# Performance work log

Measured on AMD Instinct MI355X. Metric: run time of the kernel, lower is better.

The kernel has to match this reference:

```python
import jax, jax.numpy as jnp
import numpy as np

B, T, N = 32, 512, 16
C, V, D, H, L = 150, 832, 512, 512, 5  # chord vocab, note vocab, embed dim, hidden, layers


def setup_inputs() -> dict:
    key = jax.random.key(0)
    ks = jax.random.split(key, 16)
    s = 0.05
    note = jax.random.randint(ks[0], (B, T, N), 0, V)
    chord = jax.random.randint(ks[1], (B, T), 0, C)
    chord_table = jax.random.normal(ks[2], (C, D), jnp.float32) * s
    note_table = jax.random.normal(ks[3], (V, D), jnp.float32) * s
    # GRU layer 0 (input = 2*D), layers 1..L-1 (input = H), gate order r,z,n like torch
    w_ih0 = jax.random.normal(ks[4], (3 * H, 2 * D), jnp.float32) * s
    w_hh0 = jax.random.normal(ks[5], (3 * H, H), jnp.float32) * s
    b_ih0 = jax.random.normal(ks[6], (3 * H,), jnp.float32) * s
    b_hh0 = jax.random.normal(ks[7], (3 * H,), jnp.float32) * s
    w_ih_r = jax.random.normal(ks[8], (L - 1, 3 * H, H), jnp.float32) * s
    w_hh_r = jax.random.normal(ks[9], (L - 1, 3 * H, H), jnp.float32) * s
    b_ih_r = jax.random.normal(ks[10], (L - 1, 3 * H), jnp.float32) * s
    b_hh_r = jax.random.normal(ks[11], (L - 1, 3 * H), jnp.float32) * s
    fc_w = jax.random.normal(ks[12], (C, H), jnp.float32) * s
    fc_b = jax.random.normal(ks[13], (C,), jnp.float32) * s
    return dict(note=note, chord=chord, chord_table=chord_table, note_table=note_table,
                w_ih0=w_ih0, w_hh0=w_hh0, b_ih0=b_ih0, b_hh0=b_hh0,
                w_ih_r=w_ih_r, w_hh_r=w_hh_r, b_ih_r=b_ih_r, b_hh_r=b_hh_r,
                fc_w=fc_w, fc_b=fc_b)


def _gru_layer(x, wih, whh, bih, bhh):
    # x: [B, T, in] -> [B, T, H], torch GRU cell math (gate order r,z,n)
    xp = jnp.einsum('bti,gi->btg', x, wih) + bih          # precompute input proj [B,T,3H]
    xp = jnp.swapaxes(xp, 0, 1)                            # [T,B,3H]
    h0 = jnp.zeros((x.shape[0], whh.shape[1]), x.dtype)

    def step(h, xpt):
        gh = h @ whh.T + bhh
        xr, xz, xn = jnp.split(xpt, 3, axis=-1)
        hr, hz, hn = jnp.split(gh, 3, axis=-1)
        r = jax.nn.sigmoid(xr + hr)
        z = jax.nn.sigmoid(xz + hz)
        n = jnp.tanh(xn + r * hn)
        h_new = (1.0 - z) * n + z * h
        return h_new, h_new

    _, ys = jax.lax.scan(step, h0, xp)
    return jnp.swapaxes(ys, 0, 1)                          # [B,T,H]


def _forward(note, chord, chord_table, note_table, w_ih0, w_hh0, b_ih0, b_hh0,
             w_ih_r, w_hh_r, b_ih_r, b_hh_r, fc_w, fc_b):
    # padding_idx=0: zero row 0 of both tables (also blocks its gradient)
    ct = chord_table.at[0].set(0.0)
    nt = note_table.at[0].set(0.0)
    chord_emb = ct[chord]                                   # [B,T,D]
    # ragged mean over notes before first zero; mask[k]=1 iff no zero in note[...,:k+1]
    mask = jnp.cumprod((note != 0).astype(chord_table.dtype), axis=-1)  # [B,T,N]
    emb = nt[note]                                          # [B,T,N,D]
    cnt = jnp.maximum(mask.sum(-1), 1.0)                    # zero_index==0 case -> mean of zero row
    note_emb = jnp.einsum('btnd,btn->btd', emb, mask) / cnt[..., None]
    x = jnp.concatenate([chord_emb, note_emb], axis=-1)     # [B,T,2D]
    x = _gru_layer(x, w_ih0, w_hh0, b_ih0, b_hh0)
    for l in range(w_ih_r.shape[0]):
        x = _gru_layer(x, w_ih_r[l], w_hh_r[l], b_ih_r[l], b_hh_r[l])
    return x @ fc_w.T + fc_b                                # [B,T,C]


def reference(note, chord, chord_table, note_table, w_ih0, w_hh0, b_ih0, b_hh0,
              w_ih_r, w_hh_r, b_ih_r, b_hh_r, fc_w, fc_b):
    return _forward(note, chord, chord_table, note_table, w_ih0, w_hh0, b_ih0, b_hh0,
                    w_ih_r, w_hh_r, b_ih_r, b_hh_r, fc_w, fc_b)
```

## Files before the change

### kernel.cpp

```cpp
#include <hip/hip_runtime.h>
#include <hip/hip_bf16.h>

#define B_   32
#define T_   512
#define NN_  16
#define CV_  150
#define D_   512
#define H_   512
#define BT_  16384
#define K0_  1024
#define G3H_ 1536
#define NBF_ 160
#define GXB_ 6144
#define FCB_ 768
#define XSLOT_ 16384
#define XRING_ 32
#define HRING_ 8
#define SENT32 0x7f7f7f7fu
#define HCAP 16384
#define XCAP 16384
#define BCAP 65536

using bf16x8 = __attribute__((ext_vector_type(8))) short;
using f32x4  = __attribute__((ext_vector_type(4))) float;
using u32x4  = __attribute__((ext_vector_type(4))) unsigned int;
typedef unsigned long long u64;

__device__ __forceinline__ unsigned short f2bf(float f){
  unsigned int u = __builtin_bit_cast(unsigned int, f);
  u += 0x7fffu + ((u >> 16) & 1u);
  return (unsigned short)(u >> 16);
}

__device__ __forceinline__ void store8(unsigned short* p, f32x4 a, f32x4 b){
  union { unsigned short us[8]; u32x4 v; } u;
  u.us[0]=f2bf(a[0]); u.us[1]=f2bf(a[1]); u.us[2]=f2bf(a[2]); u.us[3]=f2bf(a[3]);
  u.us[4]=f2bf(b[0]); u.us[5]=f2bf(b[1]); u.us[6]=f2bf(b[2]); u.us[7]=f2bf(b[3]);
  *(u32x4*)p = u.v;
}

__device__ __forceinline__ u64 ld_coh_u64(const u64* p){
  return __hip_atomic_load(p, __ATOMIC_RELAXED, __HIP_MEMORY_SCOPE_AGENT);
}
__device__ __forceinline__ void st_coh_u32(void* p, unsigned int v){
  __hip_atomic_store((unsigned int*)p, v, __ATOMIC_RELAXED, __HIP_MEMORY_SCOPE_AGENT);
}
__device__ __forceinline__ float ld_coh_f32(const float* p){
  return __hip_atomic_load(p, __ATOMIC_RELAXED, __HIP_MEMORY_SCOPE_AGENT);
}
__device__ __forceinline__ void st_coh_f32(float* p, float v){
  __hip_atomic_store((unsigned int*)p, __builtin_bit_cast(unsigned int, v),
                     __ATOMIC_RELAXED, __HIP_MEMORY_SCOPE_AGENT);
}
__device__ __forceinline__ void st_flag(int* p, int v){
  __hip_atomic_store(p, v, __ATOMIC_RELAXED, __HIP_MEMORY_SCOPE_AGENT);
}
__device__ __forceinline__ int ld_flag(const int* p){
  return __hip_atomic_load(p, __ATOMIC_RELAXED, __HIP_MEMORY_SCOPE_AGENT);
}

__device__ __forceinline__ bool bad64(u64 q){
  return ((unsigned int)q == SENT32) | ((unsigned int)(q >> 32) == SENT32);
}

__global__ void convert_bf16(const float* __restrict__ src,
                             unsigned short* __restrict__ dst, int n){
  int i = blockIdx.x * 256 + threadIdx.x;
  if (i < n) dst[i] = f2bf(src[i]);
}

__global__ __launch_bounds__(64) void emb_kernel(
    const int* __restrict__ note, const int* __restrict__ chord,
    const float* __restrict__ ctab, const float* __restrict__ ntab,
    unsigned short* __restrict__ x0){
  const int bt = blockIdx.x;
  const int tid = threadIdx.x;
  __shared__ int sn[NN_];
  if (tid < NN_) sn[tid] = note[bt * NN_ + tid];
  __syncthreads();
  float alive = 1.f, cnt = 0.f;
  float msk[NN_];
  #pragma unroll
  for (int k = 0; k < NN_; ++k){ if (sn[k] == 0) alive = 0.f; msk[k] = alive; cnt += alive; }
  const float inv = 1.f / fmaxf(cnt, 1.f);
  const int ch = chord[bt];
  const int d0 = tid * 8;
  f32x4 c0 = {0.f,0.f,0.f,0.f}, c1 = {0.f,0.f,0.f,0.f};
  if (ch != 0){
    const float* cp = ctab + (size_t)ch * D_ + d0;
    c0 = *(const f32x4*)cp; c1 = *(const f32x4*)(cp + 4);
  }
  f32x4 s0 = {0.f,0.f,0.f,0.f}, s1 = {0.f,0.f,0.f,0.f};
  #pragma unroll
  for (int k = 0; k < NN_; ++k){
    if (msk[k] != 0.f){
      const float* np = ntab + (size_t)sn[k] * D_ + d0;
      s0 += *(const f32x4*)np;
      s1 += *(const f32x4*)(np + 4);
    }
  }
  s0 *= inv; s1 *= inv;
  unsigned short* o = x0 + (size_t)bt * K0_ + d0;
  store8(o, c0, c1);
  store8(o + D_, s0, s1);
}

union Ufrag { u64 q[2]; bf16x8 v; };

__global__ __launch_bounds__(256, 1) void gru_fused(
    float* xp, unsigned short* hT, unsigned short* xT, unsigned short* xout,
    int* cprog, const unsigned short* __restrict__ x0g,
    const unsigned short* __restrict__ wih0g, const float* __restrict__ bih0g,
    int* gprog,
    const float* __restrict__ whh0g, const float* __restrict__ whhrg,
    const float* __restrict__ wihrg, const float* __restrict__ bhh0g,
    const float* __restrict__ bihrg, const float* __restrict__ bhhrg,
    int* l4prog, const unsigned short* __restrict__ fcwbg,
    const float* __restrict__ fcbg, float* outg){
  __shared__ unsigned short w_s[96 * 512];
  __shared__ float p_s[2][4][2][2][16][16];

  const int tid = threadIdx.x;
  const int blk = blockIdx.x;

  if (blk >= NBF_ && blk < NBF_ + GXB_){
    const int idx = blk - NBF_;
    const int gx  = idx % 24;
    const int gyy = idx / 24;
    const int bb  = gyy & 31, tc = gyy >> 5;
    const int m0  = bb * 512 + tc * 64;
    const int lane = tid & 63, wave = tid >> 6;
    const int l15 = lane & 15, kq4 = lane >> 4;
    const int m_frag = m0 + wave * 16 + l15;
    const int n_base = gx * 64;
    f32x4 acc[4] = {{0.f,0.f,0.f,0.f},{0.f,0.f,0.f,0.f},{0.f,0.f,0.f,0.f},{0.f,0.f,0.f,0.f}};
    const unsigned short* xptr = x0g + (size_t)m_frag * K0_ + kq4 * 8;
    const unsigned short* wptr[4];
    #pragma unroll
    for (int i = 0; i < 4; ++i){
      int n = n_base + i * 16 + l15;
      wptr[i] = wih0g + (size_t)n * K0_ + kq4 * 8;
    }
    for (int k0 = 0; k0 < K0_; k0 += 32){
      bf16x8 a = *(const bf16x8*)(xptr + k0);
      #pragma unroll
      for (int i = 0; i < 4; ++i){
        bf16x8 b = *(const bf16x8*)(wptr[i] + k0);
        acc[i] = __builtin_amdgcn_mfma_f32_16x16x32_bf16(a, b, acc[i], 0, 0, 0);
      }
    }
    const int mrow = m0 + wave * 16 + kq4 * 4;
    #pragma unroll
    for (int i = 0; i < 4; ++i){
      int n = n_base + i * 16 + l15;
      float bv = bih0g[n];
      #pragma unroll
      for (int r = 0; r < 4; ++r){
        int m = mrow + r;
        float v = acc[i][r] + bv;
        st_coh_f32(&xp[((size_t)(m & (T_-1)) * G3H_ + n) * B_ + (m >> 9)], v);
      }
    }
    asm volatile("s_waitcnt vmcnt(0)" ::: "memory");
    __syncthreads();
    if (tid == 0) atomicAdd(&gprog[tc], 1);
    return;
  }

  if (blk >= NBF_ + GXB_){
    const int fidx = blk - NBF_ - GXB_;
    const int fx  = fidx % 3;
    const int fyy = fidx / 3;
    const int bb  = fyy & 31, tmc = fyy >> 5;
    const int m0  = bb * 512 + tmc * 64;
    const int lane = tid & 63, wave = tid >> 6;
    const int l15 = lane & 15, kq4 = lane >> 4;
    const int need = tmc * 64 + 63;
    {
      int itc = 0;
      while (true){
        int v = (lane < 32) ? ld_flag(&l4prog[lane]) : 0x7fffffff;
        if (__all(v >= need)) break;
        if (++itc > (1 << 20)) break;
        __builtin_amdgcn_s_sleep(8);
      }
    }
    __builtin_amdgcn_sched_barrier(0);
    const int m_frag = m0 + wave * 16 + l15;
    f32x4 acc[4] = {{0.f,0.f,0.f,0.f},{0.f,0.f,0.f,0.f},{0.f,0.f,0.f,0.f},{0.f,0.f,0.f,0.f}};
    const unsigned short* xptr = xout + (size_t)m_frag * H_ + kq4 * 8;
    const unsigned short* wptr[4];
    #pragma unroll
    for (int i = 0; i < 4; ++i){
      int n = fx * 64 + i * 16 + l15;
      if (n >= CV_) n = CV_ - 1;
      wptr[i] = fcwbg + (size_t)n * H_ + kq4 * 8;
    }
    for (int k0 = 0; k0 < H_; k0 += 32){
      Ufrag ua;
      const u64* sp = (const u64*)(xptr + k0);
      ua.q[0] = ld_coh_u64(sp); ua.q[1] = ld_coh_u64(sp + 1);
      bf16x8 a = ua.v;
      #pragma unroll
      for (int i = 0; i < 4; ++i){
        bf16x8 b = *(const bf16x8*)(wptr[i] + k0);
        acc[i] = __builtin_amdgcn_mfma_f32_16x16x32_bf16(a, b, acc[i], 0, 0, 0);
      }
    }
    const int mrow = m0 + wave * 16 + kq4 * 4;
    #pragma unroll
    for (int i = 0; i < 4; ++i){
      int n = fx * 64 + i * 16 + l15;
      if (n < CV_){
        float bv = fcbg[n];
        #pragma unroll
        for (int r = 0; r < 4; ++r)
          outg[(size_t)(mrow + r) * CV_ + n] = acc[i][r] + bv;
      }
    }
    return;
  }

  const int l   = blk >> 5;
  const int sub = blk & 31;

  {
    #pragma unroll 1
    for (int i = 0; i < 24; ++i){
      int idx = i * 256 + tid;
      int fr = idx >> 6, lam = idx & 63;
      int ks = fr & 31, g = fr >> 5;
      int row = g * 512 + sub * 16 + (lam & 15);
      int kcol = (ks & 15) * 32 + ((lam >> 4) << 3);
      f32x4 a = {0.f,0.f,0.f,0.f}, b2 = {0.f,0.f,0.f,0.f};
      if (l == 0){
        if (ks < 16){
          const float* sp = whh0g + (size_t)row * H_ + kcol;
          a = *(const f32x4*)sp; b2 = *(const f32x4*)(sp + 4);
        }
      } else {
        const float* wbase = (ks < 16) ? whhrg : wihrg;
        const float* sp = wbase + (size_t)(l - 1) * G3H_ * H_ + (size_t)row * H_ + kcol;
        a = *(const f32x4*)sp; b2 = *(const f32x4*)(sp + 4);
      }
      store8(&w_s[fr * 512 + lam * 8], a, b2);
    }
  }
  __syncthreads();

  const int lane = tid & 63, wave = tid >> 6;
  const int l15 = lane & 15, l4 = lane >> 4;
  const int myn = wave >> 1;
  const int kh  = wave & 1;
  const int myb = (myn << 4) + l15;
  const int fro = (l4 << 3);
  const int khofs = kh * 256;
  const int khb = kh * 8;

  const int cb = tid & 31;
  const int cj = (tid >> 5) * 2;
  const int jg = sub * 16 + cj;

  float br0, bz0, bx0, bn0, br1, bz1, bx1, bn1;
  if (l == 0){
    br0 = bhh0g[jg];       bz0 = bhh0g[512 + jg];     bx0 = 0.f; bn0 = bhh0g[1024 + jg];
    br1 = bhh0g[jg + 1];   bz1 = bhh0g[512 + jg + 1]; bx1 = 0.f; bn1 = bhh0g[1024 + jg + 1];
  } else {
    const float* bi = bihrg + (size_t)(l - 1) * G3H_;
    const float* bh = bhhrg + (size_t)(l - 1) * G3H_;
    br0 = bi[jg] + bh[jg];           bz0 = bi[512 + jg] + bh[512 + jg];
    bx0 = bi[1024 + jg];             bn0 = bh[1024 + jg];
    br1 = bi[jg + 1] + bh[jg + 1];   bz1 = bi[512 + jg + 1] + bh[512 + jg + 1];
    bx1 = bi[1024 + jg + 1];         bn1 = bh[1024 + jg + 1];
  }
  float hres0 = 0.f, hres1 = 0.f;

  unsigned short* hTl = hT + (size_t)l * (HRING_ * 32 * 512);
  unsigned short* xTw = xT + (size_t)(l < 4 ? l : 0) * ((size_t)XRING_ * XSLOT_);
  const unsigned short* xTr = xT + (size_t)(l > 0 ? l - 1 : 0) * ((size_t)XRING_ * XSLOT_);
  const int* bp_own = cprog + (l << 5);
  int*       bp_pub = cprog + ((l > 0 ? l - 1 : 0) << 5);

  float era=0,eza=0,ena=0,era1=0,eza1=0,ena1=0;
  float erb=0,ezb=0,enb=0,erb1=0,ezb1=0,enb1=0;
  if (l == 0){
    if (tid == 0){
      int itc = 0;
      while (ld_flag(&gprog[0]) < 768){
        if (++itc > (1 << 20)) break;
        __builtin_amdgcn_s_sleep(8);
      }
    }
    __syncthreads();
    { const float* xq = xp + (size_t)0 * (G3H_ * B_) + cb;
      era=ld_coh_f32(&xq[(size_t)(0*H_+jg)*B_]); era1=ld_coh_f32(&xq[(size_t)(0*H_+jg+1)*B_]);
      eza=ld_coh_f32(&xq[(size_t)(1*H_+jg)*B_]); eza1=ld_coh_f32(&xq[(size_t)(1*H_+jg+1)*B_]);
      ena=ld_coh_f32(&xq[(size_t)(2*H_+jg)*B_]); ena1=ld_coh_f32(&xq[(size_t)(2*H_+jg+1)*B_]); }
    { const float* xq = xp + (size_t)1 * (G3H_ * B_) + cb;
      erb=ld_coh_f32(&xq[(size_t)(0*H_+jg)*B_]); erb1=ld_coh_f32(&xq[(size_t)(0*H_+jg+1)*B_]);
      ezb=ld_coh_f32(&xq[(size_t)(1*H_+jg)*B_]); ezb1=ld_coh_f32(&xq[(size_t)(1*H_+jg+1)*B_]);
      enb=ld_coh_f32(&xq[(size_t)(2*H_+jg)*B_]); enb1=ld_coh_f32(&xq[(size_t)(2*H_+jg+1)*B_]); }
  }

  for (int t = 0; t < T_; ++t){
    const int pb = t & 1;

    Ufrag xb[8];
    const unsigned short* xs = nullptr;
    if (l > 0){
      xs = xTr + (size_t)(t & (XRING_-1)) * XSLOT_ + (size_t)myb * 512 + khofs + fro;
      #pragma unroll
      for (int j = 0; j < 8; ++j){
        const u64* sp = (const u64*)(xs + (j << 5));
        xb[j].q[0] = ld_coh_u64(sp); xb[j].q[1] = ld_coh_u64(sp + 1);
      }
    }

    Ufrag hb[8];
    const unsigned short* hf = hTl + (((size_t)(t & (HRING_-1)) * 32 + myb) << 9) + khofs + fro;
    #pragma unroll
    for (int j = 0; j < 8; ++j){
      const u64* sp = (const u64*)(hf + (j << 5));
      hb[j].q[0] = ld_coh_u64(sp); hb[j].q[1] = ld_coh_u64(sp + 1);
    }

    if (l < 4 && t && (t & 3) == 0){
      int itc = 0;
      while (true){
        int v = (lane < 32) ? ld_flag(&bp_own[lane]) : 0x7fffffff;
        if (__all(v >= t - 4)) break;
        if (++itc > BCAP) break;
        __builtin_amdgcn_s_sleep(2);
      }
    }

    f32x4 accR = {0.f,0.f,0.f,0.f}, accZ = {0.f,0.f,0.f,0.f};
    f32x4 accN = {0.f,0.f,0.f,0.f}, accX = {0.f,0.f,0.f,0.f};

    if (l > 0){
      #pragma unroll
      for (int j = 0; j < 8; ++j){
        int itc = 0;
        while (__any((int)(bad64(xb[j].q[0]) | bad64(xb[j].q[1])))){
          if (++itc > XCAP) break;
          if (itc > 2) __builtin_amdgcn_s_sleep(2);
          const u64* sp = (const u64*)(xs + (j << 5));
          xb[j].q[0] = ld_coh_u64(sp); xb[j].q[1] = ld_coh_u64(sp + 1);
        }
        bf16x8 b  = xb[j].v;
        bf16x8 a0 = *(const bf16x8*)&w_s[(0 * 32 + 16 + khb + j) * 512 + lane * 8];
        bf16x8 a1 = *(const bf16x8*)&w_s[(1 * 32 + 16 + khb + j) * 512 + lane * 8];
        bf16x8 a2 = *(const bf16x8*)&w_s[(2 * 32 + 16 + khb + j) * 512 + lane * 8];
        accR = __builtin_amdgcn_mfma_f32_16x16x32_bf16(a0, b, accR, 0, 0, 0);
        accZ = __builtin_amdgcn_mfma_f32_16x16x32_bf16(a1, b, accZ, 0, 0, 0);
        accX = __builtin_amdgcn_mfma_f32_16x16x32_bf16(a2, b, accX, 0, 0, 0);
      }
    }

    #pragma unroll
    for (int j = 0; j < 8; ++j){
      int itc = 0;
      while (__any((int)(bad64(hb[j].q[0]) | bad64(hb[j].q[1])))){
        if (++itc > HCAP) break;
        if (itc > 2) __builtin_amdgcn_s_sleep(2);
        const u64* sp = (const u64*)(hf + (j << 5));
        hb[j].q[0] = ld_coh_u64(sp); hb[j].q[1] = ld_coh_u64(sp + 1);
      }
      bf16x8 b  = hb[j].v;
      bf16x8 a0 = *(const bf16x8*)&w_s[(0 * 32 + khb + j) * 512 + lane * 8];
      bf16x8 a1 = *(const bf16x8*)&w_s[(1 * 32 + khb + j) * 512 + lane * 8];
      bf16x8 a2 = *(const bf16x8*)&w_s[(2 * 32 + khb + j) * 512 + lane * 8];
      accR = __builtin_amdgcn_mfma_f32_16x16x32_bf16(a0, b, accR, 0, 0, 0);
      accZ = __builtin_amdgcn_mfma_f32_16x16x32_bf16(a1, b, accZ, 0, 0, 0);
      accN = __builtin_amdgcn_mfma_f32_16x16x32_bf16(a2, b, accN, 0, 0, 0);
    }

    float erc=0,ezc=0,enc=0,erc1=0,ezc1=0,enc1=0;
    if (l == 0){
      if (((t + 2) & 63) == 0){
        const int ck = ((t + 2) & (T_ - 1)) >> 6;
        if (tid == 0){
          int itc = 0;
          while (ld_flag(&gprog[ck]) < 768){
            if (++itc > (1 << 20)) break;
            __builtin_amdgcn_s_sleep(8);
          }
        }
        __syncthreads();
      }
      const float* xq = xp + (size_t)((t + 2) & (T_ - 1)) * (G3H_ * B_) + cb;
      erc=ld_coh_f32(&xq[(size_t)(0*H_+jg)*B_]); erc1=ld_coh_f32(&xq[(size_t)(0*H_+jg+1)*B_]);
      ezc=ld_coh_f32(&xq[(size_t)(1*H_+jg)*B_]); ezc1=ld_coh_f32(&xq[(size_t)(1*H_+jg+1)*B_]);
      enc=ld_coh_f32(&xq[(size_t)(2*H_+jg)*B_]); enc1=ld_coh_f32(&xq[(size_t)(2*H_+jg+1)*B_]);
    }

    #pragma unroll
    for (int r = 0; r < 4; ++r){
      int u = l4 * 4 + r;
      p_s[pb][0][myn][kh][u][l15] = accR[r];
      p_s[pb][1][myn][kh][u][l15] = accZ[r];
      p_s[pb][2][myn][kh][u][l15] = accN[r];
      p_s[pb][3][myn][kh][u][l15] = accX[r];
    }
    __syncthreads();

    {
      const int nt = cb >> 4, bc = cb & 15;
      float rp0 = p_s[pb][0][nt][0][cj][bc]   + p_s[pb][0][nt][1][cj][bc];
      float rp1 = p_s[pb][0][nt][0][cj+1][bc] + p_s[pb][0][nt][1][cj+1][bc];
      float zp0 = p_s[pb][1][nt][0][cj][bc]   + p_s[pb][1][nt][1][cj][bc];
      float zp1 = p_s[pb][1][nt][0][cj+1][bc] + p_s[pb][1][nt][1][cj+1][bc];
      float hp0 = p_s[pb][2][nt][0][cj][bc]   + p_s[pb][2][nt][1][cj][bc];
      float hp1 = p_s[pb][2][nt][0][cj+1][bc] + p_s[pb][2][nt][1][cj+1][bc];
      float xq0 = p_s[pb][3][nt][0][cj][bc]   + p_s[pb][3][nt][1][cj][bc];
      float xq1 = p_s[pb][3][nt][0][cj+1][bc] + p_s[pb][3][nt][1][cj+1][bc];
      float r0 = 1.f / (1.f + __expf(-(rp0 + era  + br0)));
      float r1 = 1.f / (1.f + __expf(-(rp1 + era1 + br1)));
      float z0 = 1.f / (1.f + __expf(-(zp0 + eza  + bz0)));
      float z1 = 1.f / (1.f + __expf(-(zp1 + eza1 + bz1)));
      float nx0 = (l > 0) ? (xq0 + bx0) : ena;
      float nx1 = (l > 0) ? (xq1 + bx1) : ena1;
      float e0 = __expf(2.f * (nx0 + r0 * (hp0 + bn0)));
      float e1 = __expf(2.f * (nx1 + r1 * (hp1 + bn1)));
      float n0 = (e0 - 1.f) / (e0 + 1.f);
      float n1 = (e1 - 1.f) / (e1 + 1.f);
      float h0 = (1.f - z0) * n0 + z0 * hres0; hres0 = h0;
      float h1 = (1.f - z1) * n1 + z1 * hres1; hres1 = h1;
      unsigned int pk = (unsigned int)f2bf(h0) | ((unsigned int)f2bf(h1) << 16);

      st_coh_u32(hTl + (((size_t)((t + 1) & (HRING_-1)) * 32 + cb) << 9) + jg, pk);
      if (l < 4)
        st_coh_u32(xTw + (size_t)(t & (XRING_-1)) * XSLOT_ + (size_t)cb * 512 + jg, pk);
      else
        st_coh_u32(&xout[((size_t)cb * T_ + t) * H_ + jg], pk);
      st_coh_u32(hTl + (((size_t)((t + 4) & (HRING_-1)) * 32 + cb) << 9) + jg, SENT32);
      if (l < 4)
        st_coh_u32(xTw + (size_t)((t + 16) & (XRING_-1)) * XSLOT_ + (size_t)cb * 512 + jg, SENT32);

      if (l > 0 && (t & 3) == 3 && tid == 0) st_flag(&bp_pub[sub], t);
      if (l == 4 && (t & 3) == 3 && tid == 0) st_flag(&l4prog[sub], t - 1);

      era = erb; eza = ezb; ena = enb; era1 = erb1; eza1 = ezb1; ena1 = enb1;
      erb = erc; ezb = ezc; enb = enc; erb1 = erc1; ezb1 = ezc1; enb1 = enc1;
    }
  }
  __syncthreads();
  if (l == 4 && tid == 0) st_flag(&l4prog[sub], T_ - 1);
}

extern "C" void kernel_launch(void* const* d_in, const int* in_sizes, int n_in,
                              void* d_out, int out_size, void* d_ws, size_t ws_size,
                              hipStream_t stream){
  (void)in_sizes; (void)n_in; (void)out_size; (void)ws_size;
  const int*   note  = (const int*)d_in[0];
  const int*   chord = (const int*)d_in[1];
  const float* ctab  = (const float*)d_in[2];
  const float* ntab  = (const float*)d_in[3];
  const float* wih0  = (const float*)d_in[4];
  const float* whh0  = (const float*)d_in[5];
  const float* bih0  = (const float*)d_in[6];
  const float* bhh0  = (const float*)d_in[7];
  const float* wihr  = (const float*)d_in[8];
  const float* whhr  = (const float*)d_in[9];
  const float* bihr  = (const float*)d_in[10];
  const float* bhhr  = (const float*)d_in[11];
  const float* fcw   = (const float*)d_in[12];
  const float* fcb   = (const float*)d_in[13];
  float* out = (float*)d_out;

  char* ws = (char*)d_ws;
  size_t off = 0;
  auto alloc = [&](size_t bytes)->char*{
    char* p = ws + off; off = (off + bytes + 255) & ~(size_t)255; return p;
  };
  int*            cprog   = (int*)alloc(160 * sizeof(int));
  int*            gprog   = (int*)alloc(8 * sizeof(int));
  int*            l4prog  = (int*)alloc(32 * sizeof(int));
  float*          xp      = (float*)alloc((size_t)BT_ * G3H_ * 4);
  unsigned short* fcw_b   = (unsigned short*)alloc((size_t)CV_ * H_ * 2);
  unsigned short* xout    = (unsigned short*)alloc((size_t)BT_ * H_ * 2);
  unsigned short* x0      = (unsigned short*)alloc((size_t)BT_ * K0_ * 2);
  unsigned short* wih0_b  = (unsigned short*)alloc((size_t)G3H_ * K0_ * 2);
  const size_t hT_bytes = (size_t)5 * HRING_ * 32 * 512 * 2;
  const size_t xT_bytes = (size_t)4 * XRING_ * XSLOT_ * 2;
  unsigned short* hT      = (unsigned short*)alloc(hT_bytes);
  unsigned short* xT      = (unsigned short*)alloc(xT_bytes);

  hipMemsetAsync(cprog, 0, 160 * sizeof(int), stream);
  hipMemsetAsync(gprog, 0, 8 * sizeof(int), stream);
  hipMemsetAsync(l4prog, 0xFF, 32 * sizeof(int), stream);
  hipMemsetAsync(hT, 0x7F, hT_bytes, stream);
  for (int ll = 0; ll < 5; ++ll)
    hipMemsetAsync(hT + (size_t)ll * (HRING_ * 32 * 512), 0, 32 * 512 * 2, stream);
  hipMemsetAsync(xT, 0x7F, xT_bytes, stream);

  { int n = G3H_ * K0_; convert_bf16<<<(n + 255) / 256, 256, 0, stream>>>(wih0, wih0_b, n); }
  { int n = CV_ * H_;   convert_bf16<<<(n + 255) / 256, 256, 0, stream>>>(fcw, fcw_b, n); }

  emb_kernel<<<BT_, 64, 0, stream>>>(note, chord, ctab, ntab, x0);

  gru_fused<<<NBF_ + GXB_ + FCB_, 256, 0, stream>>>(
      xp, hT, xT, xout, cprog, x0, wih0_b, bih0, gprog,
      whh0, whhr, wihr, bhh0, bihr, bhhr, l4prog, fcw_b, fcb, out);
}
```

Measured before the change: 5.414 ms.

## Move final FC projection out of fused GRU kernel into separate GEMM launch

Removes the 768 FC blocks that spin-waited on layer-4 progress flags inside the persistent fused kernel and runs the output projection as a standalone bf16 MFMA GEMM after the GRU kernel finishes. Layer-4 output stores become plain stores and the l4prog flag publishing is dropped. This avoids the spinning FC blocks competing with the recurrent blocks and the extra coherent stores and flags. The cost is that the FC work can no longer overlap the tail of the recurrence and needs an extra kernel launch.

```diff
diff --git a/kernel.cpp b/kernel.cpp
--- a/kernel.cpp
+++ b/kernel.cpp
@@ -12,7 +12,6 @@
 #define G3H_ 1536
 #define NBF_ 160
 #define GXB_ 6144
-#define FCB_ 768
 #define XSLOT_ 16384
 #define XRING_ 32
 #define HRING_ 8
@@ -105,6 +104,49 @@
   store8(o + D_, s0, s1);
 }
 
+__global__ __launch_bounds__(256) void gemm_bt(
+    const unsigned short* __restrict__ X, const unsigned short* __restrict__ W,
+    const float* __restrict__ bias, float* __restrict__ Y,
+    int M, int N, int K, int wmode){
+  const int lane = threadIdx.x & 63;
+  const int wave = threadIdx.x >> 6;
+  const int l15 = lane & 15, kq4 = lane >> 4;
+  const int m_frag = blockIdx.y * 64 + wave * 16 + l15;
+  const int n_base = blockIdx.x * 64;
+  f32x4 acc[4] = {{0.f,0.f,0.f,0.f},{0.f,0.f,0.f,0.f},{0.f,0.f,0.f,0.f},{0.f,0.f,0.f,0.f}};
+  const unsigned short* xptr = X + (size_t)m_frag * K + kq4 * 8;
+  const unsigned short* wptr[4];
+  #pragma unroll
+  for (int i = 0; i < 4; ++i){
+    int n = n_base + i * 16 + l15;
+    if (n >= N) n = N - 1;
+    wptr[i] = W + (size_t)n * K + kq4 * 8;
+  }
+  for (int k0 = 0; k0 < K; k0 += 32){
+    bf16x8 a = *(const bf16x8*)(xptr + k0);
+    #pragma unroll
+    for (int i = 0; i < 4; ++i){
+      bf16x8 b = *(const bf16x8*)(wptr[i] + k0);
+      acc[i] = __builtin_amdgcn_mfma_f32_16x16x32_bf16(a, b, acc[i], 0, 0, 0);
+    }
+  }
+  const int mrow = blockIdx.y * 64 + wave * 16 + kq4 * 4;
+  #pragma unroll
+  for (int i = 0; i < 4; ++i){
+    int n = n_base + i * 16 + l15;
+    if (n < N){
+      float bv = bias[n];
+      #pragma unroll
+      for (int r = 0; r < 4; ++r){
+        int m = mrow + r;
+        float v = acc[i][r] + bv;
+        if (wmode == 0) Y[(size_t)m * N + n] = v;
+        else            Y[((size_t)(m & (T_-1)) * N + n) * B_ + (m >> 9)] = v;
+      }
+    }
+  }
+}
+
 union Ufrag { u64 q[2]; bf16x8 v; };
 
 __global__ __launch_bounds__(256, 1) void gru_fused(
@@ -114,16 +156,14 @@
     int* gprog,
     const float* __restrict__ whh0g, const float* __restrict__ whhrg,
     const float* __restrict__ wihrg, const float* __restrict__ bhh0g,
-    const float* __restrict__ bihrg, const float* __restrict__ bhhrg,
-    int* l4prog, const unsigned short* __restrict__ fcwbg,
-    const float* __restrict__ fcbg, float* outg){
+    const float* __restrict__ bihrg, const float* __restrict__ bhhrg){
   __shared__ unsigned short w_s[96 * 512];
   __shared__ float p_s[2][4][2][2][16][16];
 
   const int tid = threadIdx.x;
   const int blk = blockIdx.x;
 
-  if (blk >= NBF_ && blk < NBF_ + GXB_){
+  if (blk >= NBF_){
     const int idx = blk - NBF_;
     const int gx  = idx % 24;
     const int gyy = idx / 24;
@@ -164,60 +204,6 @@
     asm volatile("s_waitcnt vmcnt(0)" ::: "memory");
     __syncthreads();
     if (tid == 0) atomicAdd(&gprog[tc], 1);
-    return;
-  }
-
-  if (blk >= NBF_ + GXB_){
-    const int fidx = blk - NBF_ - GXB_;
-    const int fx  = fidx % 3;
-    const int fyy = fidx / 3;
-    const int bb  = fyy & 31, tmc = fyy >> 5;
-    const int m0  = bb * 512 + tmc * 64;
-    const int lane = tid & 63, wave = tid >> 6;
-    const int l15 = lane & 15, kq4 = lane >> 4;
-    const int need = tmc * 64 + 63;
-    {
-      int itc = 0;
-      while (true){
-        int v = (lane < 32) ? ld_flag(&l4prog[lane]) : 0x7fffffff;
-        if (__all(v >= need)) break;
-        if (++itc > (1 << 20)) break;
-        __builtin_amdgcn_s_sleep(8);
-      }
-    }
-    __builtin_amdgcn_sched_barrier(0);
-    const int m_frag = m0 + wave * 16 + l15;
-    f32x4 acc[4] = {{0.f,0.f,0.f,0.f},{0.f,0.f,0.f,0.f},{0.f,0.f,0.f,0.f},{0.f,0.f,0.f,0.f}};
-    const unsigned short* xptr = xout + (size_t)m_frag * H_ + kq4 * 8;
-    const unsigned short* wptr[4];
-    #pragma unroll
-    for (int i = 0; i < 4; ++i){
-      int n = fx * 64 + i * 16 + l15;
-      if (n >= CV_) n = CV_ - 1;
-      wptr[i] = fcwbg + (size_t)n * H_ + kq4 * 8;
-    }
-    for (int k0 = 0; k0 < H_; k0 += 32){
-      Ufrag ua;
-      const u64* sp = (const u64*)(xptr + k0);
-      ua.q[0] = ld_coh_u64(sp); ua.q[1] = ld_coh_u64(sp + 1);
-      bf16x8 a = ua.v;
-      #pragma unroll
-      for (int i = 0; i < 4; ++i){
-        bf16x8 b = *(const bf16x8*)(wptr[i] + k0);
-        acc[i] = __builtin_amdgcn_mfma_f32_16x16x32_bf16(a, b, acc[i], 0, 0, 0);
-      }
-    }
-    const int mrow = m0 + wave * 16 + kq4 * 4;
-    #pragma unroll
-    for (int i = 0; i < 4; ++i){
-      int n = fx * 64 + i * 16 + l15;
-      if (n < CV_){
-        float bv = fcbg[n];
-        #pragma unroll
-        for (int r = 0; r < 4; ++r)
-          outg[(size_t)(mrow + r) * CV_ + n] = acc[i][r] + bv;
-      }
-    }
     return;
   }
 
@@ -432,20 +418,17 @@
       if (l < 4)
         st_coh_u32(xTw + (size_t)(t & (XRING_-1)) * XSLOT_ + (size_t)cb * 512 + jg, pk);
       else
-        st_coh_u32(&xout[((size_t)cb * T_ + t) * H_ + jg], pk);
+        *(unsigned int*)&xout[((size_t)cb * T_ + t) * H_ + jg] = pk;
       st_coh_u32(hTl + (((size_t)((t + 4) & (HRING_-1)) * 32 + cb) << 9) + jg, SENT32);
       if (l < 4)
         st_coh_u32(xTw + (size_t)((t + 16) & (XRING_-1)) * XSLOT_ + (size_t)cb * 512 + jg, SENT32);
 
       if (l > 0 && (t & 3) == 3 && tid == 0) st_flag(&bp_pub[sub], t);
-      if (l == 4 && (t & 3) == 3 && tid == 0) st_flag(&l4prog[sub], t - 1);
 
       era = erb; eza = ezb; ena = enb; era1 = erb1; eza1 = ezb1; ena1 = enb1;
       erb = erc; ezb = ezc; enb = enc; erb1 = erc1; ezb1 = ezc1; enb1 = enc1;
     }
   }
-  __syncthreads();
-  if (l == 4 && tid == 0) st_flag(&l4prog[sub], T_ - 1);
 }
 
 extern "C" void kernel_launch(void* const* d_in, const int* in_sizes, int n_in,
@@ -475,7 +458,6 @@
   };
   int*            cprog   = (int*)alloc(160 * sizeof(int));
   int*            gprog   = (int*)alloc(8 * sizeof(int));
-  int*            l4prog  = (int*)alloc(32 * sizeof(int));
   float*          xp      = (float*)alloc((size_t)BT_ * G3H_ * 4);
   unsigned short* fcw_b   = (unsigned short*)alloc((size_t)CV_ * H_ * 2);
   unsigned short* xout    = (unsigned short*)alloc((size_t)BT_ * H_ * 2);
@@ -488,7 +470,6 @@
 
   hipMemsetAsync(cprog, 0, 160 * sizeof(int), stream);
   hipMemsetAsync(gprog, 0, 8 * sizeof(int), stream);
-  hipMemsetAsync(l4prog, 0xFF, 32 * sizeof(int), stream);
   hipMemsetAsync(hT, 0x7F, hT_bytes, stream);
   for (int ll = 0; ll < 5; ++ll)
     hipMemsetAsync(hT + (size_t)ll * (HRING_ * 32 * 512), 0, 32 * 512 * 2, stream);
@@ -499,7 +480,10 @@
 
   emb_kernel<<<BT_, 64, 0, stream>>>(note, chord, ctab, ntab, x0);
 
-  gru_fused<<<NBF_ + GXB_ + FCB_, 256, 0, stream>>>(
+  gru_fused<<<NBF_ + GXB_, 256, 0, stream>>>(
       xp, hT, xT, xout, cprog, x0, wih0_b, bih0, gprog,
-      whh0, whhr, wihr, bhh0, bihr, bhhr, l4prog, fcw_b, fcb, out);
-}
+      whh0, whhr, wihr, bhh0, bihr, bhhr);
+
+  gemm_bt<<<dim3((CV_ + 63) / 64, BT_ / 64), 256, 0, stream>>>(
+      xout, fcw_b, fcb, out, BT_, CV_, H_, 0);
+}
```

New measurement: 5.434 ms. About the same (+0.4%).
